# Performance work log

Measured on AMD Instinct MI355X. Metric: run time of the kernel, lower is better.

## Reference

```python
import jax, jax.numpy as jnp
import numpy as np

RES = 0.16      # config.resolution (m)
XMIN = -51.2    # config.x_min
YMIN = -51.2    # config.y_min
EPS = 1e-5      # BatchNorm eps
NEG = -1.0e9


def setup_inputs() -> dict:
    key = jax.random.key(0)
    ks = jax.random.split(key, 12)
    P, M = 100000, 32
    C_IN, C_MID, C_OUT = 9, 64, 64
    pillars = jax.random.normal(ks[0], (P, M, 4), dtype=jnp.float32)
    pillar_coords = jax.random.randint(ks[1], (P, 2), 0, 640, dtype=jnp.int64)
    num_points_per_pillar = jax.random.randint(ks[2], (P,), 0, 33, dtype=jnp.int64)
    # MLP params (Linear stored as (in,out) for x @ W + b)
    W1 = jax.random.normal(ks[3], (C_IN, C_MID), dtype=jnp.float32) / np.sqrt(C_IN)
    b1 = jax.random.normal(ks[4], (C_MID,), dtype=jnp.float32) * 0.01
    g1 = jnp.ones((C_MID,), jnp.float32)
    beta1 = jnp.zeros((C_MID,), jnp.float32)
    m1 = jax.random.normal(ks[5], (C_MID,), dtype=jnp.float32) * 0.1
    v1 = jax.random.uniform(ks[6], (C_MID,), dtype=jnp.float32, minval=0.5, maxval=1.5)
    W2 = jax.random.normal(ks[7], (C_MID, C_OUT), dtype=jnp.float32) / np.sqrt(C_MID)
    b2 = jax.random.normal(ks[8], (C_OUT,), dtype=jnp.float32) * 0.01
    g2 = jnp.ones((C_OUT,), jnp.float32)
    beta2 = jnp.zeros((C_OUT,), jnp.float32)
    m2 = jax.random.normal(ks[9], (C_OUT,), dtype=jnp.float32) * 0.1
    v2 = jax.random.uniform(ks[10], (C_OUT,), dtype=jnp.float32, minval=0.5, maxval=1.5)
    return {
        "pillars": pillars, "pillar_coords": pillar_coords,
        "num_points_per_pillar": num_points_per_pillar,
        "W1": W1, "b1": b1, "g1": g1, "beta1": beta1, "m1": m1, "v1": v1,
        "W2": W2, "b2": b2, "g2": g2, "beta2": beta2, "m2": m2, "v2": v2,
    }


def reference(pillars, pillar_coords, num_points_per_pillar,
              W1, b1, g1, beta1, m1, v1, W2, b2, g2, beta2, m2, v2):
    P, M, _ = pillars.shape
    # pillar centers from grid indices
    xc = (pillar_coords[:, 1].astype(jnp.float32) + 0.5) * RES + XMIN  # (P,)
    yc = (pillar_coords[:, 0].astype(jnp.float32) + 0.5) * RES + YMIN  # (P,)
    npts = num_points_per_pillar.astype(jnp.float32)
    mask = (jnp.arange(M)[None, :] < num_points_per_pillar[:, None]).astype(pillars.dtype)  # (P,M)
    x, y, z, r = pillars[:, :, 0], pillars[:, :, 1], pillars[:, :, 2], pillars[:, :, 3]
    z_mean = (z * mask).sum(axis=1) / jnp.clip(npts, 1.0)  # (P,)
    xo = x - xc[:, None]
    yo = y - yc[:, None]
    zo = z - z_mean[:, None]
    feat = jnp.stack([x, y, z, r, xo, yo, zo, xo, yo], axis=-1)  # (P,M,9)
    # shared MLP: Linear -> BN(eval) -> ReLU, twice
    h = feat @ W1 + b1
    h = jax.nn.relu(g1 * (h - m1) * jax.lax.rsqrt(v1 + EPS) + beta1)
    h = h @ W2 + b2
    h = jax.nn.relu(g2 * (h - m2) * jax.lax.rsqrt(v2 + EPS) + beta2)  # (P,M,64)
    # masked max over points per pillar
    m3 = mask[:, :, None]
    h = h * m3 + (1.0 - m3) * NEG
    return h.max(axis=1)  # (P,64)
```

## Files before the change

### kernel.cpp

```cpp
#include <hip/hip_runtime.h>
#include <type_traits>

#define RES_ 0.16f
#define XMIN_ -51.2f
#define YMIN_ -51.2f
#define EPS_ 1e-5f
#define NEG_ -1000000000.0f

#define WPB 4

typedef _Float16 f16x8 __attribute__((ext_vector_type(8)));
typedef _Float16 f16x4 __attribute__((ext_vector_type(4)));
typedef _Float16 f16x2 __attribute__((ext_vector_type(2)));
typedef float f32x4 __attribute__((ext_vector_type(4)));

union F8u { f16x8 v; f16x2 h[4]; };
union F4u { f16x4 v; f16x2 h[2]; };

static __device__ __forceinline__ f16x2 pkrtz(float a, float b) {
    return __builtin_bit_cast(f16x2, __builtin_amdgcn_cvt_pkrtz(a, b));
}

static __device__ __forceinline__ f16x2 relu2(f16x2 x) {
#if __has_builtin(__builtin_elementwise_max)
    const f16x2 z2 = (f16x2)(_Float16)0.f;
    return __builtin_elementwise_max(x, z2);
#else
    f16x2 r;
    r[0] = x[0] > (_Float16)0.f ? x[0] : (_Float16)0.f;
    r[1] = x[1] > (_Float16)0.f ? x[1] : (_Float16)0.f;
    return r;
#endif
}

static __device__ __forceinline__ float fast_rcp(float x) {
#if __has_builtin(__builtin_amdgcn_rcpf)
    return __builtin_amdgcn_rcpf(x);
#else
    return 1.0f / x;
#endif
}

template <int CTRL>
static __device__ __forceinline__ float dpp_ror_add(float x) {
    int r = __builtin_amdgcn_update_dpp(0, __float_as_int(x), CTRL, 0xf, 0xf, true);
    return x + __int_as_float(r);
}

static __device__ __forceinline__ float xmax16(float x) {
    float a = x, b = x;
    asm("v_permlane16_swap_b32 %0, %1" : "+v"(a), "+v"(b));
    return fmaxf(a, b);
}
static __device__ __forceinline__ float xmax32(float x) {
    float a = x, b = x;
    asm("v_permlane32_swap_b32 %0, %1" : "+v"(a), "+v"(b));
    return fmaxf(a, b);
}

template <int IDX0, int IDX1>
static __device__ __forceinline__ void lds_read2_b128(unsigned base, f16x8& a, f16x8& b) {
    asm volatile("ds_read_b128 %0, %2 offset:%c3\n\t"
                 "ds_read_b128 %1, %2 offset:%c4\n\t"
                 "s_waitcnt lgkmcnt(0)"
                 : "=v"(a), "=v"(b)
                 : "v"(base), "i"(IDX0 * 1024), "i"(IDX1 * 1024));
}

__global__ __launch_bounds__(256, 5) void pfn_kernel(
    const float* __restrict__ pillars,
    const int* __restrict__ coords,
    const int* __restrict__ npts_arr,
    const float* __restrict__ W1, const float* __restrict__ b1,
    const float* __restrict__ g1, const float* __restrict__ beta1,
    const float* __restrict__ m1, const float* __restrict__ v1,
    const float* __restrict__ W2, const float* __restrict__ b2,
    const float* __restrict__ g2, const float* __restrict__ beta2,
    const float* __restrict__ m2, const float* __restrict__ v2,
    float* __restrict__ out, int P)
{
    const int tid  = threadIdx.x;
    const int wave = tid >> 6;
    const int lane = tid & 63;
    const int quad = lane >> 4;
    const int col  = lane & 15;

    __shared__ _Float16 bw2s[8][64][8];

    {
        const int nt = wave;
        const int n0 = nt * 16 + col;
        const float a2 = g2[n0] * rsqrtf(v2[n0] + EPS_);
#pragma unroll
        for (int kt = 0; kt < 2; ++kt) {
            F8u w;
#pragma unroll
            for (int j = 0; j < 8; ++j) {
                const int c = 32 * kt + 16 * (j >> 2) + 4 * quad + (j & 3);
                w.v[j] = (_Float16)(a2 * W2[c * 64 + n0]);
            }
            *(f16x8*)&bw2s[kt * 4 + nt][lane][0] = w.v;
        }
    }

    f16x4 aw1[4];
#pragma unroll
    for (int mt = 0; mt < 4; ++mt) {
        const int ch = mt * 16 + col;
        const float a1 = g1[ch] * rsqrtf(v1[ch] + EPS_);
        const float c1 = fmaf(a1, b1[ch] - m1[ch], beta1[ch]);
#pragma unroll
        for (int j = 0; j < 4; ++j) {
            const int k = quad * 4 + j;
            float w;
            if (k < 9)        w = a1 * W1[k * 64 + ch];
            else if (k == 9)  w = c1;
            else if (k == 10) w = a1 * W1[6 * 64 + ch];
            else              w = 0.0f;
            aw1[mt][j] = (_Float16)w;
        }
    }
    const float c2own = fmaf(g2[lane] * rsqrtf(v2[lane] + EPS_),
                             b2[lane] - m2[lane], beta2[lane]);

    __syncthreads();

    const unsigned bwbase = (unsigned)(size_t)&bw2s[0][lane][0];

    auto zreduce = [&](const float4& A, const float4& B, int n) -> float {
        float zs = (col < n) ? A.z : 0.0f;
        zs += (16 + col < n) ? B.z : 0.0f;
        zs = dpp_ror_add<0x128>(zs);
        zs = dpp_ror_add<0x124>(zs);
        zs = dpp_ror_add<0x122>(zs);
        zs = dpp_ror_add<0x121>(zs);
        return zs * fast_rcp(fmaxf((float)n, 1.0f));
    };

    const int nwaves = gridDim.x * WPB;
    int p = __builtin_amdgcn_readfirstlane(blockIdx.x * WPB + wave);
    if (p >= P) return;

    const float4* pb = (const float4*)(pillars + (size_t)p * 128);
    float4 ptA = pb[col];
    float4 ptB = pb[16 + col];
    int np = npts_arr[p];
    int cy = coords[2 * p], cx = coords[2 * p + 1];
    np = np < 0 ? 0 : (np > 32 ? 32 : np);
    float z_cur = zreduce(ptA, ptB, np);

    while (true) {
        const int pn = p + nwaves;
        const bool has_next = pn < P;
        float4 ptAn, ptBn; int npn = 0, cyn = 0, cxn = 0;
        if (has_next) {
            const float4* pbn = (const float4*)(pillars + (size_t)pn * 128);
            ptAn = pbn[col];
            ptBn = pbn[16 + col];
            npn = npts_arr[pn];
            cyn = coords[2 * pn]; cxn = coords[2 * pn + 1];
        }

        const int npu = __builtin_amdgcn_readfirstlane(np);
        const float xc = ((float)cx + 0.5f) * RES_ + XMIN_;
        const float yc = ((float)cy + 0.5f) * RES_ + YMIN_;
        const float z_mean = z_cur;

        auto body = [&](auto MTC) -> float {
            constexpr int MT = decltype(MTC)::value;
            float hm4[4] = {NEG_, NEG_, NEG_, NEG_};

#pragma unroll
            for (int t = 0; t < MT; ++t) {
                const float4 pt = (t == 0) ? ptA : ptB;

                const float xo = pt.x - xc;
                const float yo = pt.y - yc;
                const f16x2 c01 = pkrtz(pt.x, pt.y);
                const f16x2 c23 = pkrtz(pt.z, pt.w);
                const f16x2 c45 = pkrtz(xo, yo);
                const f16x2 c67 = pkrtz(pt.z, xo);
                const f16x2 c89 = pkrtz(yo, 1.0f);
                const f16x2 cab = pkrtz(-z_mean, 0.0f);
                const f16x2 z2  = (f16x2)(_Float16)0.f;
                F4u u;
                u.h[0] = (quad == 0) ? c01 : (quad == 1) ? c45 : (quad == 2) ? c89 : z2;
                u.h[1] = (quad == 0) ? c23 : (quad == 1) ? c67 : (quad == 2) ? cab : z2;
                const f16x4 bt = u.v;

                f32x4 acc1[4];
                const f32x4 zz = {0.f, 0.f, 0.f, 0.f};
#pragma unroll
                for (int mt = 0; mt < 4; ++mt)
                    acc1[mt] = __builtin_amdgcn_mfma_f32_16x16x16f16(aw1[mt], bt, zz, 0, 0, 0);

                f16x8 av2[2];
#pragma unroll
                for (int kt = 0; kt < 2; ++kt) {
                    F8u w;
                    w.h[0] = relu2(pkrtz(acc1[2 * kt][0],     acc1[2 * kt][1]));
                    w.h[1] = relu2(pkrtz(acc1[2 * kt][2],     acc1[2 * kt][3]));
                    w.h[2] = relu2(pkrtz(acc1[2 * kt + 1][0], acc1[2 * kt + 1][1]));
                    w.h[3] = relu2(pkrtz(acc1[2 * kt + 1][2], acc1[2 * kt + 1][3]));
                    av2[kt] = w.v;
                }

                f32x4 cm;
#pragma unroll
                for (int r = 0; r < 4; ++r)
                    cm[r] = (t * 16 + quad * 4 + r < np) ? 0.0f : NEG_;

                auto nts = [&](auto NTC) {
                    constexpr int nt = decltype(NTC)::value;
                    f16x8 b0, b1;
                    lds_read2_b128<nt, 4 + nt>(bwbase, b0, b1);
                    f32x4 acc = __builtin_amdgcn_mfma_f32_16x16x32_f16(av2[0], b0, cm, 0, 0, 0);
                    acc = __builtin_amdgcn_mfma_f32_16x16x32_f16(av2[1], b1, acc, 0, 0, 0);
                    hm4[nt] = fmaxf(fmaxf(hm4[nt], fmaxf(acc[0], acc[1])),
                                    fmaxf(acc[2], acc[3]));
                };
                nts(std::integral_constant<int, 0>{});
                nts(std::integral_constant<int, 1>{});
                nts(std::integral_constant<int, 2>{});
                nts(std::integral_constant<int, 3>{});
            }

            float hmv[4];
#pragma unroll
            for (int nt = 0; nt < 4; ++nt)
                hmv[nt] = xmax32(xmax16(hm4[nt]));
            float r0 = (quad == 0) ? hmv[0] : (quad == 1) ? hmv[1] : (quad == 2) ? hmv[2] : hmv[3];
            return fmaxf(r0 + c2own, 0.0f);
        };

        float res;
        if (npu > 16)     res = body(std::integral_constant<int, 2>{});
        else if (npu > 0) res = body(std::integral_constant<int, 1>{});
        else              res = NEG_;
        out[(size_t)p * 64 + lane] = res;

        if (!has_next) break;

        npn = npn < 0 ? 0 : (npn > 32 ? 32 : npn);
        z_cur = zreduce(ptAn, ptBn, npn);

        p = pn; ptA = ptAn; ptB = ptBn; np = npn; cy = cyn; cx = cxn;
    }
}

extern "C" void kernel_launch(void* const* d_in, const int* in_sizes, int n_in,
                              void* d_out, int out_size, void* d_ws, size_t ws_size,
                              hipStream_t stream) {
    const float* pillars = (const float*)d_in[0];
    const int*   coords  = (const int*)d_in[1];
    const int*   npts    = (const int*)d_in[2];
    const float* W1      = (const float*)d_in[3];
    const float* b1      = (const float*)d_in[4];
    const float* g1      = (const float*)d_in[5];
    const float* beta1   = (const float*)d_in[6];
    const float* m1      = (const float*)d_in[7];
    const float* v1      = (const float*)d_in[8];
    const float* W2      = (const float*)d_in[9];
    const float* b2      = (const float*)d_in[10];
    const float* g2      = (const float*)d_in[11];
    const float* beta2   = (const float*)d_in[12];
    const float* m2      = (const float*)d_in[13];
    const float* v2      = (const float*)d_in[14];
    float* out           = (float*)d_out;

    const int P = in_sizes[2];
    const int blocks = 1280;

    hipLaunchKernelGGL(pfn_kernel, dim3(blocks), dim3(256), 0, stream,
                       pillars, coords, npts, W1, b1, g1, beta1, m1, v1,
                       W2, b2, g2, beta2, m2, v2, out, P);
}
```

Measured before the change: 154.3 us.

## Software-pipeline layer-1 MFMA of next pillar with layer-2 of current pillar

Restructures the persistent per-wave loop so that the first-layer MFMA and ReLU packing for the next pillar are interleaved with the second-layer MFMAs and max reduction for the current pillar. The loads prefetch two pillars ahead, and the z-mean reduction runs one pillar early. The aim is to hide MFMA and LDS latency by giving the scheduler independent work. This needs more live registers, so launch bounds drop to 4 waves per SIMD and the grid shrinks from 1280 to 1024 blocks to match, trading occupancy for instruction-level parallelism.

```diff
diff --git a/kernel.cpp b/kernel.cpp
--- a/kernel.cpp
+++ b/kernel.cpp
@@ -67,7 +67,7 @@
                  : "v"(base), "i"(IDX0 * 1024), "i"(IDX1 * 1024));
 }
 
-__global__ __launch_bounds__(256, 5) void pfn_kernel(
+__global__ __launch_bounds__(256, 4) void pfn_kernel(
     const float* __restrict__ pillars,
     const int* __restrict__ coords,
     const int* __restrict__ npts_arr,
@@ -137,114 +137,181 @@
         return zs * fast_rcp(fmaxf((float)n, 1.0f));
     };
 
+    auto Xt = [&](const float4& pt, float xcv, float ycv, float zmv,
+                  f16x8& o0, f16x8& o1) {
+        const float xo = pt.x - xcv;
+        const float yo = pt.y - ycv;
+        const f16x2 c01 = pkrtz(pt.x, pt.y);
+        const f16x2 c23 = pkrtz(pt.z, pt.w);
+        const f16x2 c45 = pkrtz(xo, yo);
+        const f16x2 c67 = pkrtz(pt.z, xo);
+        const f16x2 c89 = pkrtz(yo, 1.0f);
+        const f16x2 cab = pkrtz(-zmv, 0.0f);
+        const f16x2 z2  = (f16x2)(_Float16)0.f;
+        F4u u;
+        u.h[0] = (quad == 0) ? c01 : (quad == 1) ? c45 : (quad == 2) ? c89 : z2;
+        u.h[1] = (quad == 0) ? c23 : (quad == 1) ? c67 : (quad == 2) ? cab : z2;
+        f32x4 a0c, a1c, a2c, a3c;
+        const f32x4 zz = {0.f, 0.f, 0.f, 0.f};
+        a0c = __builtin_amdgcn_mfma_f32_16x16x16f16(aw1[0], u.v, zz, 0, 0, 0);
+        a1c = __builtin_amdgcn_mfma_f32_16x16x16f16(aw1[1], u.v, zz, 0, 0, 0);
+        a2c = __builtin_amdgcn_mfma_f32_16x16x16f16(aw1[2], u.v, zz, 0, 0, 0);
+        a3c = __builtin_amdgcn_mfma_f32_16x16x16f16(aw1[3], u.v, zz, 0, 0, 0);
+        F8u w0, w1;
+        w0.h[0] = relu2(pkrtz(a0c[0], a0c[1]));
+        w0.h[1] = relu2(pkrtz(a0c[2], a0c[3]));
+        w0.h[2] = relu2(pkrtz(a1c[0], a1c[1]));
+        w0.h[3] = relu2(pkrtz(a1c[2], a1c[3]));
+        w1.h[0] = relu2(pkrtz(a2c[0], a2c[1]));
+        w1.h[1] = relu2(pkrtz(a2c[2], a2c[3]));
+        w1.h[2] = relu2(pkrtz(a3c[0], a3c[1]));
+        w1.h[3] = relu2(pkrtz(a3c[2], a3c[3]));
+        o0 = w0.v;
+        o1 = w1.v;
+    };
+
+    auto Yt = [&](const f16x8& a0, const f16x8& a1, const f32x4& cm,
+                  float& h0, float& h1, float& h2, float& h3) {
+        f16x8 b0, b1; f32x4 acc;
+        lds_read2_b128<0, 4>(bwbase, b0, b1);
+        acc = __builtin_amdgcn_mfma_f32_16x16x32_f16(a0, b0, cm, 0, 0, 0);
+        acc = __builtin_amdgcn_mfma_f32_16x16x32_f16(a1, b1, acc, 0, 0, 0);
+        h0 = fmaxf(fmaxf(h0, fmaxf(acc[0], acc[1])), fmaxf(acc[2], acc[3]));
+        lds_read2_b128<1, 5>(bwbase, b0, b1);
+        acc = __builtin_amdgcn_mfma_f32_16x16x32_f16(a0, b0, cm, 0, 0, 0);
+        acc = __builtin_amdgcn_mfma_f32_16x16x32_f16(a1, b1, acc, 0, 0, 0);
+        h1 = fmaxf(fmaxf(h1, fmaxf(acc[0], acc[1])), fmaxf(acc[2], acc[3]));
+        lds_read2_b128<2, 6>(bwbase, b0, b1);
+        acc = __builtin_amdgcn_mfma_f32_16x16x32_f16(a0, b0, cm, 0, 0, 0);
+        acc = __builtin_amdgcn_mfma_f32_16x16x32_f16(a1, b1, acc, 0, 0, 0);
+        h2 = fmaxf(fmaxf(h2, fmaxf(acc[0], acc[1])), fmaxf(acc[2], acc[3]));
+        lds_read2_b128<3, 7>(bwbase, b0, b1);
+        acc = __builtin_amdgcn_mfma_f32_16x16x32_f16(a0, b0, cm, 0, 0, 0);
+        acc = __builtin_amdgcn_mfma_f32_16x16x32_f16(a1, b1, acc, 0, 0, 0);
+        h3 = fmaxf(fmaxf(h3, fmaxf(acc[0], acc[1])), fmaxf(acc[2], acc[3]));
+    };
+
+    auto mkcm = [&](int npv, int tt) -> f32x4 {
+        f32x4 cm;
+#pragma unroll
+        for (int r = 0; r < 4; ++r)
+            cm[r] = (tt * 16 + quad * 4 + r < npv) ? 0.0f : NEG_;
+        return cm;
+    };
+
+    auto epi = [&](float h0, float h1, float h2, float h3) -> float {
+        const float e0 = xmax32(xmax16(h0));
+        const float e1 = xmax32(xmax16(h1));
+        const float e2 = xmax32(xmax16(h2));
+        const float e3 = xmax32(xmax16(h3));
+        const float r0 = (quad == 0) ? e0 : (quad == 1) ? e1 : (quad == 2) ? e2 : e3;
+        return fmaxf(r0 + c2own, 0.0f);
+    };
+
     const int nwaves = gridDim.x * WPB;
-    int p = __builtin_amdgcn_readfirstlane(blockIdx.x * WPB + wave);
+    int p = blockIdx.x * WPB + wave;
     if (p >= P) return;
 
     const float4* pb = (const float4*)(pillars + (size_t)p * 128);
-    float4 ptA = pb[col];
-    float4 ptB = pb[16 + col];
-    int np = npts_arr[p];
-    int cy = coords[2 * p], cx = coords[2 * p + 1];
-    np = np < 0 ? 0 : (np > 32 ? 32 : np);
-    float z_cur = zreduce(ptA, ptB, np);
+    float4 cA = pb[col], cB = pb[16 + col];
+    int np_c = npts_arr[p];
+    int cy_c = coords[2 * p], cx_c = coords[2 * p + 1];
+    np_c = np_c < 0 ? 0 : (np_c > 32 ? 32 : np_c);
+    float zm_c = zreduce(cA, cB, np_c);
+    f16x8 A0, A1, B0, B1;
+    {
+        const float xcc = ((float)cx_c + 0.5f) * RES_ + XMIN_;
+        const float ycc = ((float)cy_c + 0.5f) * RES_ + YMIN_;
+        Xt(cA, xcc, ycc, zm_c, A0, A1);
+        if (__builtin_amdgcn_readfirstlane(np_c) > 16)
+            Xt(cB, xcc, ycc, zm_c, B0, B1);
+    }
+
+    int pn = p + nwaves;
+    bool hn = pn < P;
+    float4 nA{}, nB{};
+    int np_n = 0, cy_n = 0, cx_n = 0;
+    float zm_n = 0.0f;
+    if (hn) {
+        const float4* pbn = (const float4*)(pillars + (size_t)pn * 128);
+        nA = pbn[col]; nB = pbn[16 + col];
+        np_n = npts_arr[pn];
+        cy_n = coords[2 * pn]; cx_n = coords[2 * pn + 1];
+        np_n = np_n < 0 ? 0 : (np_n > 32 ? 32 : np_n);
+        zm_n = zreduce(nA, nB, np_n);
+    }
 
     while (true) {
-        const int pn = p + nwaves;
-        const bool has_next = pn < P;
-        float4 ptAn, ptBn; int npn = 0, cyn = 0, cxn = 0;
-        if (has_next) {
-            const float4* pbn = (const float4*)(pillars + (size_t)pn * 128);
-            ptAn = pbn[col];
-            ptBn = pbn[16 + col];
-            npn = npts_arr[pn];
-            cyn = coords[2 * pn]; cxn = coords[2 * pn + 1];
-        }
-
-        const int npu = __builtin_amdgcn_readfirstlane(np);
-        const float xc = ((float)cx + 0.5f) * RES_ + XMIN_;
-        const float yc = ((float)cy + 0.5f) * RES_ + YMIN_;
-        const float z_mean = z_cur;
-
-        auto body = [&](auto MTC) -> float {
-            constexpr int MT = decltype(MTC)::value;
-            float hm4[4] = {NEG_, NEG_, NEG_, NEG_};
-
-#pragma unroll
-            for (int t = 0; t < MT; ++t) {
-                const float4 pt = (t == 0) ? ptA : ptB;
-
-                const float xo = pt.x - xc;
-                const float yo = pt.y - yc;
-                const f16x2 c01 = pkrtz(pt.x, pt.y);
-                const f16x2 c23 = pkrtz(pt.z, pt.w);
-                const f16x2 c45 = pkrtz(xo, yo);
-                const f16x2 c67 = pkrtz(pt.z, xo);
-                const f16x2 c89 = pkrtz(yo, 1.0f);
-                const f16x2 cab = pkrtz(-z_mean, 0.0f);
-                const f16x2 z2  = (f16x2)(_Float16)0.f;
-                F4u u;
-                u.h[0] = (quad == 0) ? c01 : (quad == 1) ? c45 : (quad == 2) ? c89 : z2;
-                u.h[1] = (quad == 0) ? c23 : (quad == 1) ? c67 : (quad == 2) ? cab : z2;
-                const f16x4 bt = u.v;
-
-                f32x4 acc1[4];
-                const f32x4 zz = {0.f, 0.f, 0.f, 0.f};
-#pragma unroll
-                for (int mt = 0; mt < 4; ++mt)
-                    acc1[mt] = __builtin_amdgcn_mfma_f32_16x16x16f16(aw1[mt], bt, zz, 0, 0, 0);
-
-                f16x8 av2[2];
-#pragma unroll
-                for (int kt = 0; kt < 2; ++kt) {
-                    F8u w;
-                    w.h[0] = relu2(pkrtz(acc1[2 * kt][0],     acc1[2 * kt][1]));
-                    w.h[1] = relu2(pkrtz(acc1[2 * kt][2],     acc1[2 * kt][3]));
-                    w.h[2] = relu2(pkrtz(acc1[2 * kt + 1][0], acc1[2 * kt + 1][1]));
-                    w.h[3] = relu2(pkrtz(acc1[2 * kt + 1][2], acc1[2 * kt + 1][3]));
-                    av2[kt] = w.v;
-                }
-
-                f32x4 cm;
-#pragma unroll
-                for (int r = 0; r < 4; ++r)
-                    cm[r] = (t * 16 + quad * 4 + r < np) ? 0.0f : NEG_;
-
-                auto nts = [&](auto NTC) {
-                    constexpr int nt = decltype(NTC)::value;
-                    f16x8 b0, b1;
-                    lds_read2_b128<nt, 4 + nt>(bwbase, b0, b1);
-                    f32x4 acc = __builtin_amdgcn_mfma_f32_16x16x32_f16(av2[0], b0, cm, 0, 0, 0);
-                    acc = __builtin_amdgcn_mfma_f32_16x16x32_f16(av2[1], b1, acc, 0, 0, 0);
-                    hm4[nt] = fmaxf(fmaxf(hm4[nt], fmaxf(acc[0], acc[1])),
-                                    fmaxf(acc[2], acc[3]));
-                };
-                nts(std::integral_constant<int, 0>{});
-                nts(std::integral_constant<int, 1>{});
-                nts(std::integral_constant<int, 2>{});
-                nts(std::integral_constant<int, 3>{});
+        const int uc = __builtin_amdgcn_readfirstlane(np_c);
+
+        if (!hn) {
+            float res = NEG_;
+            if (uc > 0) {
+                float h0 = NEG_, h1 = NEG_, h2 = NEG_, h3 = NEG_;
+                Yt(A0, A1, mkcm(np_c, 0), h0, h1, h2, h3);
+                if (uc > 16)
+                    Yt(B0, B1, mkcm(np_c, 1), h0, h1, h2, h3);
+                res = epi(h0, h1, h2, h3);
             }
-
-            float hmv[4];
-#pragma unroll
-            for (int nt = 0; nt < 4; ++nt)
-                hmv[nt] = xmax32(xmax16(hm4[nt]));
-            float r0 = (quad == 0) ? hmv[0] : (quad == 1) ? hmv[1] : (quad == 2) ? hmv[2] : hmv[3];
-            return fmaxf(r0 + c2own, 0.0f);
+            out[(size_t)p * 64 + lane] = res;
+            break;
+        }
+
+        const int pnn = pn + nwaves;
+        const bool hnn = pnn < P;
+        float4 nnA{}, nnB{};
+        int np_nn = 0, cy_nn = 0, cx_nn = 0;
+        if (hnn) {
+            const float4* pbn = (const float4*)(pillars + (size_t)pnn * 128);
+            nnA = pbn[col]; nnB = pbn[16 + col];
+            np_nn = npts_arr[pnn];
+            cy_nn = coords[2 * pnn]; cx_nn = coords[2 * pnn + 1];
+        }
+
+        const int un = __builtin_amdgcn_readfirstlane(np_n);
+        const float xcn = ((float)cx_n + 0.5f) * RES_ + XMIN_;
+        const float ycn = ((float)cy_n + 0.5f) * RES_ + YMIN_;
+
+        f16x8 NA0, NA1, NB0, NB1;
+
+        auto yx = [&](auto MC) -> float {
+            constexpr int m = decltype(MC)::value;
+            Xt(nA, xcn, ycn, zm_n, NA0, NA1);
+            float h0 = NEG_, h1 = NEG_, h2 = NEG_, h3 = NEG_;
+            if constexpr (m >= 1) {
+                const f32x4 cm0 = mkcm(np_c, 0);
+                Yt(A0, A1, cm0, h0, h1, h2, h3);
+            }
+            if (un > 16)
+                Xt(nB, xcn, ycn, zm_n, NB0, NB1);
+            if constexpr (m == 2) {
+                const f32x4 cm1 = mkcm(np_c, 1);
+                Yt(B0, B1, cm1, h0, h1, h2, h3);
+            }
+            if constexpr (m >= 1)
+                return epi(h0, h1, h2, h3);
+            else
+                return NEG_;
         };
 
         float res;
-        if (npu > 16)     res = body(std::integral_constant<int, 2>{});
-        else if (npu > 0) res = body(std::integral_constant<int, 1>{});
-        else              res = NEG_;
+        if (uc > 16)     res = yx(std::integral_constant<int, 2>{});
+        else if (uc > 0) res = yx(std::integral_constant<int, 1>{});
+        else             res = yx(std::integral_constant<int, 0>{});
         out[(size_t)p * 64 + lane] = res;
 
-        if (!has_next) break;
-
-        npn = npn < 0 ? 0 : (npn > 32 ? 32 : npn);
-        z_cur = zreduce(ptAn, ptBn, npn);
-
-        p = pn; ptA = ptAn; ptB = ptBn; np = npn; cy = cyn; cx = cxn;
+        float zm_nn = 0.0f;
+        if (hnn) {
+            np_nn = np_nn < 0 ? 0 : (np_nn > 32 ? 32 : np_nn);
+            zm_nn = zreduce(nnA, nnB, np_nn);
+        }
+
+        p = pn; np_c = np_n;
+        A0 = NA0; A1 = NA1;
+        if (un > 16) { B0 = NB0; B1 = NB1; }
+        pn = pnn; hn = hnn;
+        nA = nnA; nB = nnB; np_n = np_nn; cy_n = cy_nn; cx_n = cx_nn;
+        zm_n = zm_nn;
     }
 }
 
@@ -269,7 +336,7 @@
     float* out           = (float*)d_out;
 
     const int P = in_sizes[2];
-    const int blocks = 1280;
+    const int blocks = 1024;
 
     hipLaunchKernelGGL(pfn_kernel, dim3(blocks), dim3(256), 0, stream,
                        pillars, coords, npts, W1, b1, g1, beta1, m1, v1,
```

Result: slower. 164.2 us (+6.4%).
